# Kernel tuning notes

Measured on AMD Instinct MI355X. Metric: run time of the kernel, lower is better.

## Reference

```python
import jax, jax.numpy as jnp
import numpy as np

B, S, E, H, V = 64, 400, 512, 512, 32000


def setup_inputs() -> dict:
    key = jax.random.key(0)
    ks = jax.random.split(key, 16)
    sc = lambda fan: 1.0 / np.sqrt(fan)
    u = lambda k, shape, fan: jax.random.uniform(k, shape, jnp.float32, -sc(fan), sc(fan))
    mask = jax.random.randint(ks[3], (B, S), 0, 2).astype(bool)
    mask = mask.at[:, 0].set(True)  # ensure at least one valid position per row
    return {
        "decoder_input": jax.random.normal(ks[0], (B, E), jnp.float32),
        "previous_hidden_state": jax.random.normal(ks[1], (B, H), jnp.float32),
        "encoder_output": jax.random.normal(ks[2], (B, S, 2 * H), jnp.float32),
        "mask": mask,
        # GRUCell params (torch layout: weight_ih [3H,E], weight_hh [3H,H])
        "w_ih": u(ks[4], (3 * H, E), H),
        "w_hh": u(ks[5], (3 * H, H), H),
        "b_ih": u(ks[6], (3 * H,), H),
        "b_hh": u(ks[7], (3 * H,), H),
        # Attention params
        "Wh_w": u(ks[8], (H, 2 * H), 2 * H),
        "Wh_b": u(ks[9], (H,), 2 * H),
        "Ws_w": u(ks[10], (H, H), H),
        "Ws_b": u(ks[11], (H,), H),
        "vatt_w": u(ks[12], (1, H), H),  # Linear(H,1,bias=False)
        # Output projections
        "V_w": u(ks[13], (H, 3 * H), 3 * H),
        "V_b": u(ks[13], (H,), 3 * H),
        "Vhat_w": u(ks[14], (V, H), H),
        "Vhat_b": u(ks[15], (V,), H),
    }


def reference(decoder_input, previous_hidden_state, encoder_output, mask,
              w_ih, w_hh, b_ih, b_hh, Wh_w, Wh_b, Ws_w, Ws_b, vatt_w,
              V_w, V_b, Vhat_w, Vhat_b):
    # --- GRUCell step (torch semantics) ---
    gi = decoder_input @ w_ih.T + b_ih                  # [B, 3H]
    gh = previous_hidden_state @ w_hh.T + b_hh          # [B, 3H]
    i_r, i_z, i_n = jnp.split(gi, 3, axis=-1)
    h_r, h_z, h_n = jnp.split(gh, 3, axis=-1)
    r = jax.nn.sigmoid(i_r + h_r)
    z = jax.nn.sigmoid(i_z + h_z)
    n = jnp.tanh(i_n + r * h_n)
    hidden = (1.0 - z) * n + z * previous_hidden_state  # [B, H]

    # --- Additive (Bahdanau) attention ---
    feat = jnp.tanh(encoder_output @ Wh_w.T + Wh_b
                    + (hidden @ Ws_w.T + Ws_b)[:, None, :])   # [B, S, H]
    scores = jnp.einsum('bsh,h->bs', feat, vatt_w[0])          # [B, S]
    scores = jnp.where(mask, scores, -jnp.inf)
    attn_dist = jax.nn.softmax(scores, axis=-1)                # [B, S]

    # --- Context + output projection ---
    context_vector = jnp.einsum('bs,bsd->bd', attn_dist, encoder_output)  # [B, 2H]
    out = jnp.concatenate([hidden, context_vector], axis=-1) @ V_w.T + V_b  # [B, H]
    logits = out @ Vhat_w.T + Vhat_b                                        # [B, V]
    vocab_dist = jax.nn.softmax(logits, axis=-1)
    return (vocab_dist, attn_dist, context_vector, hidden)
```

## Files before the change

### kernel.cpp

```cpp
#include <hip/hip_runtime.h>
#include <hip/hip_bf16.h>
#include <stdint.h>

#define DI __device__ __forceinline__

using f32x4 = __attribute__((ext_vector_type(4))) float;
using s16x8 = __attribute__((ext_vector_type(8))) short;

#define BB 64
#define SS 400
#define HH 512
#define VVOC 32000
#define MTOT (BB*SS)

DI short bf16r(float f){
  __hip_bfloat16 h = __float2bfloat16(f);
  union { __hip_bfloat16 h; short s; } u; u.h = h; return u.s;
}
DI float sigm(float x){ return 1.f/(1.f + __expf(-x)); }
DI float tanhfast(float x){ x = fminf(x, 12.f); float e = __expf(2.f*x); return (e-1.f)/(e+1.f); }

DI void gload16b(const __hip_bfloat16* g, short* l){
  __builtin_amdgcn_global_load_lds(
      (const __attribute__((address_space(1))) __hip_bfloat16*)g,
      (__attribute__((address_space(3))) short*)l, 16, 0, 0);
}

DI float blkmax(float v, float* red, int t){
  #pragma unroll
  for (int o = 32; o; o >>= 1) v = fmaxf(v, __shfl_xor(v, o));
  if ((t & 63) == 0) red[t >> 6] = v;
  __syncthreads();
  v = fmaxf(fmaxf(red[0], red[1]), fmaxf(red[2], red[3]));
  __syncthreads();
  return v;
}
DI float blksum(float v, float* red, int t){
  #pragma unroll
  for (int o = 32; o; o >>= 1) v += __shfl_xor(v, o);
  if ((t & 63) == 0) red[t >> 6] = v;
  __syncthreads();
  v = red[0] + red[1] + red[2] + red[3];
  __syncthreads();
  return v;
}

DI s16x8 cvt8(const float* src){
  f32x4 a = ((const f32x4*)src)[0];
  f32x4 b = ((const f32x4*)src)[1];
  s16x8 o;
  o[0]=bf16r(a[0]); o[1]=bf16r(a[1]); o[2]=bf16r(a[2]); o[3]=bf16r(a[3]);
  o[4]=bf16r(b[0]); o[5]=bf16r(b[1]); o[6]=bf16r(b[2]); o[7]=bf16r(b[3]);
  return o;
}

DI s16x8 fragload16(const short* tile, int rbase, int kk, int l){
  int r = rbase + (l & 15);
  int c = (kk >> 3) + (l >> 4);
  int slot = c ^ (r & 7);
  return *(const s16x8*)(tile + r*64 + slot*8);
}

__global__ __launch_bounds__(256) void cvt_all(
    const float* __restrict__ enc, const float* __restrict__ wh,
    short* __restrict__ enc16, short* __restrict__ wh16,
    const unsigned int* __restrict__ mask, int mwords, int* __restrict__ flags)
{
  int b = blockIdx.x, t = threadIdx.x;
  if (b < 1600) {
    int i = b*256 + t;
    #pragma unroll
    for (int k = 0; k < 8; ++k) {
      int idx = i + k*409600;
      ((s16x8*)enc16)[idx] = cvt8(enc + (size_t)idx*8);
    }
  } else if (b < 1856) {
    int i = (b-1600)*256 + t;
    ((s16x8*)wh16)[i] = cvt8(wh + (size_t)i*8);
  } else {
    __shared__ int f;
    if (t == 0) f = 0;
    __syncthreads();
    int loc = 0;
    for (int i = (b-1856)*256 + t; i < mwords; i += 8*256) loc |= (mask[i] > 1u) ? 1 : 0;
    if (loc) atomicOr(&f, 1);
    __syncthreads();
    if (t == 0) flags[b-1856] = f;
  }
}

__global__ __launch_bounds__(256) void mfma_small(
    const float* __restrict__ A0, const float* __restrict__ A1,
    const float* __restrict__ W0, const float* __restrict__ W1,
    float* __restrict__ P0, float* __restrict__ P1,
    int K, int N)
{
  const float* A = blockIdx.z ? A1 : A0;
  const float* W = blockIdx.z ? W1 : W0;
  float*       P = blockIdx.z ? P1 : P0;
  __shared__ __align__(16) short lsa[64*64];
  __shared__ __align__(16) short lsb[64*64];
  const int t = threadIdx.x, l = t & 63, w = t >> 6;
  const int c0 = blockIdx.x*64;
  const int kbeg = blockIdx.y*64;

  #pragma unroll
  for (int q = 0; q < 2; ++q) {
    int it = q*256 + t;
    int r = it >> 3, c = it & 7;
    int slot = (c ^ (r & 7)) << 3;
    *(s16x8*)(lsa + r*64 + slot) = cvt8(A + (size_t)r*K + kbeg + c*8);
    *(s16x8*)(lsb + r*64 + slot) = cvt8(W + (size_t)(c0 + r)*K + kbeg + c*8);
  }
  __syncthreads();

  f32x4 acc[4];
  #pragma unroll
  for (int m = 0; m < 4; ++m) { f32x4 z = {0.f,0.f,0.f,0.f}; acc[m] = z; }
  #pragma unroll
  for (int kk = 0; kk < 64; kk += 32) {
    s16x8 bf = fragload16(lsb, w*16, kk, l);
    #pragma unroll
    for (int m = 0; m < 4; ++m) {
      s16x8 af = fragload16(lsa, m*16, kk, l);
      acc[m] = __builtin_amdgcn_mfma_f32_16x16x32_bf16(af, bf, acc[m], 0, 0, 0);
    }
  }
  const int kq = l >> 4, lc = l & 15;
  const int col = c0 + w*16 + lc;
  size_t pbase = (size_t)blockIdx.y * 64 * N;
  #pragma unroll
  for (int m = 0; m < 4; ++m)
    #pragma unroll
    for (int j = 0; j < 4; ++j)
      P[pbase + (size_t)(m*16 + kq*4 + j)*N + col] = acc[m][j];
}

__global__ __launch_bounds__(256) void score_gemm_bf16(
    const __hip_bfloat16* __restrict__ A, const __hip_bfloat16* __restrict__ Bw,
    const float* __restrict__ qv, const float* __restrict__ vb, float* __restrict__ dst)
{
  __shared__ __align__(16) short lsa[128*64];
  __shared__ __align__(16) short lsb[128*64];
  const int t = threadIdx.x;
  const int l = t & 63;
  const int w = t >> 6;
  const int wm = w >> 1, wn = w & 1;
  const int phys = blockIdx.x;
  const int logical = (phys & 7)*100 + (phys >> 3);
  const int mrow = (logical >> 2) * 128;
  const int colb = logical & 3;
  const int ncol = colb * 128;

  f32x4 acc[4][4];
  #pragma unroll
  for (int m = 0; m < 4; ++m)
    #pragma unroll
    for (int n = 0; n < 4; ++n) { f32x4 z = {0.f,0.f,0.f,0.f}; acc[m][n] = z; }

  for (int k0 = 0; k0 < 1024; k0 += 64) {
    #pragma unroll
    for (int i = 0; i < 4; ++i) {
      int ci = i*256 + t;
      int r = ci >> 3;
      int slot = ci & 7;
      int c = slot ^ (r & 7);
      gload16b(A + (size_t)(mrow + r)*1024 + k0 + c*8, lsa + ci*8);
      gload16b(Bw + (size_t)(ncol + r)*1024 + k0 + c*8, lsb + ci*8);
    }
    __syncthreads();
    #pragma unroll
    for (int kk = 0; kk < 64; kk += 32) {
      s16x8 bf[4];
      #pragma unroll
      for (int n = 0; n < 4; ++n) bf[n] = fragload16(lsb, wn*64 + n*16, kk, l);
      #pragma unroll
      for (int m = 0; m < 4; ++m) {
        s16x8 af = fragload16(lsa, wm*64 + m*16, kk, l);
        #pragma unroll
        for (int n = 0; n < 4; ++n)
          acc[m][n] = __builtin_amdgcn_mfma_f32_16x16x32_bf16(af, bf[n], acc[m][n], 0, 0, 0);
      }
    }
    __syncthreads();
  }

  const int kq = l >> 4, lc = l & 15;
  float vv[4];
  #pragma unroll
  for (int n = 0; n < 4; ++n) vv[n] = vb[ncol + wn*64 + n*16 + lc];
  #pragma unroll
  for (int m = 0; m < 4; ++m) {
    #pragma unroll
    for (int j = 0; j < 4; ++j) {
      int r = mrow + wm*64 + m*16 + kq*4 + j;
      int b = r / SS;
      const float* qb = qv + b*HH + ncol + wn*64 + lc;
      float ps = 0.f;
      #pragma unroll
      for (int n = 0; n < 4; ++n) ps += vv[n]*tanhfast(acc[m][n][j] + qb[n*16]);
      #pragma unroll
      for (int o = 1; o < 16; o <<= 1) ps += __shfl_xor(ps, o);
      if (lc == 0) dst[(colb*2 + wn)*MTOT + r] = ps;
    }
  }
}

__global__ __launch_bounds__(256) void vocab_gemm(
    const float* __restrict__ OUTm, const float* __restrict__ Vhat,
    const float* __restrict__ Vb, float* __restrict__ logits,
    float* __restrict__ MAXP, float* __restrict__ SUMP)
{
  __shared__ __align__(16) short lsa[64*64];
  __shared__ __align__(16) short lsb[64*64];
  __shared__ float red[64][8];
  const int t = threadIdx.x, l = t & 63, w = t >> 6;
  const int vrow0 = blockIdx.x * 64;

  f32x4 acc[4];
  #pragma unroll
  for (int m = 0; m < 4; ++m) { f32x4 z = {0.f,0.f,0.f,0.f}; acc[m] = z; }

  for (int k0 = 0; k0 < 512; k0 += 64) {
    #pragma unroll
    for (int q = 0; q < 2; ++q) {
      int it = q*256 + t;
      int r = it >> 3, c = it & 7;
      s16x8 o = cvt8(OUTm + (size_t)r*512 + k0 + c*8);
      *(s16x8*)(lsa + r*64 + ((c ^ (r & 7)) << 3)) = o;
    }
    #pragma unroll
    for (int q = 0; q < 2; ++q) {
      int it = q*256 + t;
      int r = it >> 3, c = it & 7;
      s16x8 o = cvt8(Vhat + (size_t)(vrow0 + r)*512 + k0 + c*8);
      *(s16x8*)(lsb + r*64 + ((c ^ (r & 7)) << 3)) = o;
    }
    __syncthreads();
    #pragma unroll
    for (int kk = 0; kk < 64; kk += 32) {
      s16x8 bf = fragload16(lsb, w*16, kk, l);
      #pragma unroll
      for (int m = 0; m < 4; ++m) {
        s16x8 af = fragload16(lsa, m*16, kk, l);
        acc[m] = __builtin_amdgcn_mfma_f32_16x16x32_bf16(af, bf, acc[m], 0, 0, 0);
      }
    }
    __syncthreads();
  }

  const int kq = l >> 4, lc = l & 15;
  const int voc = vrow0 + w*16 + lc;
  const float bias = Vb[voc];
  #pragma unroll
  for (int m = 0; m < 4; ++m)
    #pragma unroll
    for (int j = 0; j < 4; ++j) {
      acc[m][j] += bias;
      int brow = m*16 + kq*4 + j;
      logits[(size_t)brow*VVOC + voc] = acc[m][j];
    }
  #pragma unroll
  for (int m = 0; m < 4; ++m)
    #pragma unroll
    for (int j = 0; j < 4; ++j) {
      float v = acc[m][j];
      #pragma unroll
      for (int o = 1; o < 16; o <<= 1) v = fmaxf(v, __shfl_xor(v, o));
      if (lc == 0) red[m*16 + kq*4 + j][w] = v;
    }
  __syncthreads();
  float gmax[4][4];
  #pragma unroll
  for (int m = 0; m < 4; ++m)
    #pragma unroll
    for (int j = 0; j < 4; ++j) {
      int row = m*16 + kq*4 + j;
      gmax[m][j] = fmaxf(fmaxf(red[row][0], red[row][1]), fmaxf(red[row][2], red[row][3]));
    }
  __syncthreads();
  #pragma unroll
  for (int m = 0; m < 4; ++m)
    #pragma unroll
    for (int j = 0; j < 4; ++j) {
      float s = __expf(acc[m][j] - gmax[m][j]);
      #pragma unroll
      for (int o = 1; o < 16; o <<= 1) s += __shfl_xor(s, o);
      if (lc == 0) red[m*16 + kq*4 + j][4 + w] = s;
    }
  __syncthreads();
  if (t < 64) {
    float M = fmaxf(fmaxf(red[t][0], red[t][1]), fmaxf(red[t][2], red[t][3]));
    float S = red[t][4] + red[t][5] + red[t][6] + red[t][7];
    MAXP[blockIdx.x*64 + t] = M;
    SUMP[blockIdx.x*64 + t] = S;
  }
}

__global__ __launch_bounds__(256) void vnorm(
    const float* __restrict__ MAXP, const float* __restrict__ SUMP,
    float* __restrict__ logits)
{
  __shared__ float red[4];
  int b = blockIdx.x, q = blockIdx.y, t = threadIdx.x;
  float m = -INFINITY;
  for (int i = t; i < 500; i += 256) m = fmaxf(m, MAXP[i*64 + b]);
  m = blkmax(m, red, t);
  float z = 0.f;
  for (int i = t; i < 500; i += 256) z += SUMP[i*64 + b] * __expf(MAXP[i*64 + b] - m);
  z = blksum(z, red, t);
  float inv = 1.f / z;
  f32x4* p = (f32x4*)(logits + (size_t)b*VVOC + q*8000);
  for (int i = t; i < 2000; i += 256) {
    f32x4 v = p[i];
    #pragma unroll
    for (int c = 0; c < 4; ++c) v[c] = __expf(v[c] - m) * inv;
    p[i] = v;
  }
}

__global__ void combineN(const float* __restrict__ P, const float* __restrict__ b1,
                         const float* __restrict__ b2, float* __restrict__ dstv,
                         int N, int total, int nseg)
{
  int i = blockIdx.x*256 + threadIdx.x;
  if (i >= total) return;
  float a = 0.f;
  for (int s = 0; s < nseg; ++s) a += P[(size_t)s*total + i];
  int c = i % N;
  if (b1) a += b1[c];
  if (b2) a += b2[c];
  dstv[i] = a;
}

__global__ void gru_gate(const float* __restrict__ GI, const float* __restrict__ GH,
                         const float* __restrict__ b_ih, const float* __restrict__ b_hh,
                         const float* __restrict__ hprev, float* __restrict__ hid,
                         float* __restrict__ concat)
{
  int i = blockIdx.x*256 + threadIdx.x;
  int b = i >> 9, h = i & 511;
  float ir=0, iz=0, inn=0, hr=0, hz=0, hn=0;
  #pragma unroll
  for (int s = 0; s < 8; ++s) {
    const float* gi = GI + (size_t)s*(64*1536) + b*1536;
    const float* gh = GH + (size_t)s*(64*1536) + b*1536;
    ir += gi[h];      iz += gi[512+h];  inn += gi[1024+h];
    hr += gh[h];      hz += gh[512+h];  hn  += gh[1024+h];
  }
  ir += b_ih[h]; iz += b_ih[512+h]; inn += b_ih[1024+h];
  hr += b_hh[h]; hz += b_hh[512+h]; hn  += b_hh[1024+h];
  float r = sigm(ir + hr), z = sigm(iz + hz);
  float n = tanhfast(inn + r*hn);
  float hv = (1.f - z)*n + z*hprev[i];
  hid[i] = hv;
  concat[b*1536 + h] = hv;
}

__global__ void softmax_s(const float* __restrict__ part, const void* __restrict__ mask,
                          const int* __restrict__ flags, float* __restrict__ attn)
{
  __shared__ float red[4];
  int b = blockIdx.x, t = threadIdx.x;
  bool isbyte = (flags[0]|flags[1]|flags[2]|flags[3]|flags[4]|flags[5]|flags[6]|flags[7]) != 0;
  float sc0, sc1 = -INFINITY;
  {
    float v = 0.f;
    #pragma unroll
    for (int p = 0; p < 8; ++p) v += part[p*MTOT + b*SS + t];
    bool mv = isbyte ? (((const unsigned char*)mask)[b*SS + t] != 0)
                     : (((const int*)mask)[b*SS + t] != 0);
    sc0 = mv ? v : -INFINITY;
  }
  int s1 = t + 256;
  if (s1 < SS) {
    float v = 0.f;
    #pragma unroll
    for (int p = 0; p < 8; ++p) v += part[p*MTOT + b*SS + s1];
    bool mv = isbyte ? (((const unsigned char*)mask)[b*SS + s1] != 0)
                     : (((const int*)mask)[b*SS + s1] != 0);
    sc1 = mv ? v : -INFINITY;
  }
  float mx = blkmax(fmaxf(sc0, sc1), red, t);
  float e0 = __expf(sc0 - mx), e1 = __expf(sc1 - mx);
  float sum = blksum(e0 + e1, red, t);
  float inv = 1.f / sum;
  attn[b*SS + t] = e0 * inv;
  if (s1 < SS) attn[b*SS + s1] = e1 * inv;
}

__global__ void ctx_part(const float* __restrict__ attn, const unsigned int* __restrict__ enc16,
                         float* __restrict__ CTXP)
{
  int b = blockIdx.x, dh = blockIdx.y, sq = blockIdx.z;
  int d0 = dh*512 + threadIdx.x*2;
  const float* a = attn + b*SS + sq*50;
  const unsigned int* e = enc16 + (((size_t)(b*SS + sq*50)*1024 + d0) >> 1);
  float lo = 0.f, hi = 0.f;
  #pragma unroll 5
  for (int s = 0; s < 50; ++s) {
    unsigned int u = e[(size_t)s*512];
    float av = a[s];
    lo += av * __uint_as_float(u << 16);
    hi += av * __uint_as_float(u & 0xffff0000u);
  }
  float* dst = CTXP + (size_t)sq*65536 + b*1024 + d0;
  dst[0] = lo; dst[1] = hi;
}

__global__ void ctx_combine(const float* __restrict__ CTXP, float* __restrict__ ctx,
                            float* __restrict__ concat)
{
  int b = blockIdx.x;
  for (int d = threadIdx.x; d < 1024; d += 256) {
    float s = 0.f;
    #pragma unroll
    for (int q = 0; q < 8; ++q) s += CTXP[q*65536 + b*1024 + d];
    ctx[b*1024 + d] = s;
    concat[b*1536 + 512 + d] = s;
  }
}

extern "C" void kernel_launch(void* const* d_in, const int* in_sizes, int n_in,
                              void* d_out, int out_size, void* d_ws, size_t ws_size,
                              hipStream_t stream) {
  (void)in_sizes; (void)n_in; (void)out_size; (void)ws_size;
  const float* x      = (const float*)d_in[0];
  const float* hprev  = (const float*)d_in[1];
  const float* enc    = (const float*)d_in[2];
  const void*  mask   = d_in[3];
  const float* w_ih   = (const float*)d_in[4];
  const float* w_hh   = (const float*)d_in[5];
  const float* b_ih   = (const float*)d_in[6];
  const float* b_hh   = (const float*)d_in[7];
  const float* Wh_w   = (const float*)d_in[8];
  const float* Wh_b   = (const float*)d_in[9];
  const float* Ws_w   = (const float*)d_in[10];
  const float* Ws_b   = (const float*)d_in[11];
  const float* vatt   = (const float*)d_in[12];
  const float* V_w    = (const float*)d_in[13];
  const float* V_b    = (const float*)d_in[14];
  const float* Vhat_w = (const float*)d_in[15];
  const float* Vhat_b = (const float*)d_in[16];

  float* out   = (float*)d_out;
  float* vocab = out;
  float* attn  = out + 2048000;
  float* ctx   = out + 2073600;
  float* hid   = out + 2139136;

  float* WS     = (float*)d_ws;
  int*   FLAGS  = (int*)d_ws;
  float* GI     = WS + 16;
  float* GH     = GI + 786432;
  float* QP     = GH + 786432;
  float* Q      = QP + 262144;
  float* OUT    = Q + 32768;
  float* PART   = OUT + 32768;
  float* MAXP   = PART + 204800;
  float* SUMP   = MAXP + 32000;
  float* CTXP   = SUMP + 32000;
  float* OUTP   = CTXP + 524288;
  float* CONCAT = OUTP + 786432;
  float* ENDF   = CONCAT + 98304;
  size_t f32_bytes = ((size_t)((char*)ENDF - (char*)d_ws) + 15) & ~(size_t)15;
  short* ENC16 = (short*)((char*)d_ws + f32_bytes);
  short* WH16  = ENC16 + (size_t)25600*1024;

  cvt_all<<<dim3(1864), 256, 0, stream>>>(enc, Wh_w, ENC16, WH16,
                                          (const unsigned int*)mask, 6400, FLAGS);
  mfma_small<<<dim3(24, 8, 2), 256, 0, stream>>>(x, hprev, w_ih, w_hh, GI, GH, 512, 1536);
  gru_gate<<<dim3(128), 256, 0, stream>>>(GI, GH, b_ih, b_hh, hprev, hid, CONCAT);
  mfma_small<<<dim3(8, 8, 1), 256, 0, stream>>>(hid, hid, Ws_w, Ws_w, QP, QP, 512, 512);
  combineN<<<dim3(128), 256, 0, stream>>>(QP, Ws_b, Wh_b, Q, 512, 32768, 8);
  score_gemm_bf16<<<dim3(800), 256, 0, stream>>>(
      (const __hip_bfloat16*)ENC16, (const __hip_bfloat16*)WH16, Q, vatt, PART);
  softmax_s<<<dim3(64), 256, 0, stream>>>(PART, mask, FLAGS, attn);
  ctx_part<<<dim3(64, 2, 8), 256, 0, stream>>>(attn, (const unsigned int*)ENC16, CTXP);
  ctx_combine<<<dim3(64), 256, 0, stream>>>(CTXP, ctx, CONCAT);
  mfma_small<<<dim3(8, 24, 1), 256, 0, stream>>>(CONCAT, CONCAT, V_w, V_w, OUTP, OUTP, 1536, 512);
  combineN<<<dim3(128), 256, 0, stream>>>(OUTP, V_b, nullptr, OUT, 512, 32768, 24);
  vocab_gemm<<<dim3(500), 256, 0, stream>>>(OUT, Vhat_w, Vhat_b, vocab, MAXP, SUMP);
  vnorm<<<dim3(64, 4), 256, 0, stream>>>(MAXP, SUMP, vocab);
}
```

Baseline: 157.8 us.

## Fuse pre-GEMMs into conversion kernel, fuse GRU gate with query, widen score tiles

Folds the GRU input/hidden GEMMs into the bf16 conversion launch as extra blocks, and merges the GRU gate and the Ws query projection into one per-batch kernel that computes the query with fp32 dot products from shared memory. The score GEMM now uses 512-thread blocks with 128x256 tiles so each encoder tile is reused across more columns. The vocab GEMM register-prefetches the next K slice before converting the current one. Together these cut kernel launches and global round trips. The cost is more LDS and registers in the score kernel, and a fused_hidq grid of only 64 blocks.

```diff
diff --git a/kernel.cpp b/kernel.cpp
--- a/kernel.cpp
+++ b/kernel.cpp
@@ -45,13 +45,14 @@
   return v;
 }
 
-DI s16x8 cvt8(const float* src){
-  f32x4 a = ((const f32x4*)src)[0];
-  f32x4 b = ((const f32x4*)src)[1];
+DI s16x8 cvt8v(f32x4 a, f32x4 b){
   s16x8 o;
   o[0]=bf16r(a[0]); o[1]=bf16r(a[1]); o[2]=bf16r(a[2]); o[3]=bf16r(a[3]);
   o[4]=bf16r(b[0]); o[5]=bf16r(b[1]); o[6]=bf16r(b[2]); o[7]=bf16r(b[3]);
   return o;
+}
+DI s16x8 cvt8(const float* src){
+  return cvt8v(((const f32x4*)src)[0], ((const f32x4*)src)[1]);
 }
 
 DI s16x8 fragload16(const short* tile, int rbase, int kk, int l){
@@ -61,11 +62,52 @@
   return *(const s16x8*)(tile + r*64 + slot*8);
 }
 
-__global__ __launch_bounds__(256) void cvt_all(
+DI void mfma_small_body(const float* __restrict__ A, const float* __restrict__ W,
+                        float* __restrict__ P, int K, int N, int c0, int kseg,
+                        short* lsa, short* lsb, int t)
+{
+  const int kbeg = kseg*64;
+  const int l = t & 63, w = t >> 6;
+  #pragma unroll
+  for (int q = 0; q < 2; ++q) {
+    int it = q*256 + t;
+    int r = it >> 3, c = it & 7;
+    int slot = (c ^ (r & 7)) << 3;
+    *(s16x8*)(lsa + r*64 + slot) = cvt8(A + (size_t)r*K + kbeg + c*8);
+    *(s16x8*)(lsb + r*64 + slot) = cvt8(W + (size_t)(c0 + r)*K + kbeg + c*8);
+  }
+  __syncthreads();
+  f32x4 acc[4];
+  #pragma unroll
+  for (int m = 0; m < 4; ++m) { f32x4 z = {0.f,0.f,0.f,0.f}; acc[m] = z; }
+  #pragma unroll
+  for (int kk = 0; kk < 64; kk += 32) {
+    s16x8 bf = fragload16(lsb, w*16, kk, l);
+    #pragma unroll
+    for (int m = 0; m < 4; ++m) {
+      s16x8 af = fragload16(lsa, m*16, kk, l);
+      acc[m] = __builtin_amdgcn_mfma_f32_16x16x32_bf16(af, bf, acc[m], 0, 0, 0);
+    }
+  }
+  const int kq = l >> 4, lc = l & 15;
+  const int col = c0 + w*16 + lc;
+  size_t pbase = (size_t)kseg * 64 * N;
+  #pragma unroll
+  for (int m = 0; m < 4; ++m)
+    #pragma unroll
+    for (int j = 0; j < 4; ++j)
+      P[pbase + (size_t)(m*16 + kq*4 + j)*N + col] = acc[m][j];
+}
+
+__global__ __launch_bounds__(256) void k_pre(
     const float* __restrict__ enc, const float* __restrict__ wh,
     short* __restrict__ enc16, short* __restrict__ wh16,
-    const unsigned int* __restrict__ mask, int mwords, int* __restrict__ flags)
-{
+    const unsigned int* __restrict__ mask, int mwords, int* __restrict__ flags,
+    const float* __restrict__ x, const float* __restrict__ hprev,
+    const float* __restrict__ w_ih, const float* __restrict__ w_hh,
+    float* __restrict__ GI, float* __restrict__ GH)
+{
+  __shared__ __align__(16) short ls[2][64*64];
   int b = blockIdx.x, t = threadIdx.x;
   if (b < 1600) {
     int i = b*256 + t;
@@ -77,7 +119,7 @@
   } else if (b < 1856) {
     int i = (b-1600)*256 + t;
     ((s16x8*)wh16)[i] = cvt8(wh + (size_t)i*8);
-  } else {
+  } else if (b < 1864) {
     __shared__ int f;
     if (t == 0) f = 0;
     __syncthreads();
@@ -86,71 +128,73 @@
     if (loc) atomicOr(&f, 1);
     __syncthreads();
     if (t == 0) flags[b-1856] = f;
-  }
-}
-
-__global__ __launch_bounds__(256) void mfma_small(
-    const float* __restrict__ A0, const float* __restrict__ A1,
-    const float* __restrict__ W0, const float* __restrict__ W1,
-    float* __restrict__ P0, float* __restrict__ P1,
-    int K, int N)
-{
-  const float* A = blockIdx.z ? A1 : A0;
-  const float* W = blockIdx.z ? W1 : W0;
-  float*       P = blockIdx.z ? P1 : P0;
-  __shared__ __align__(16) short lsa[64*64];
-  __shared__ __align__(16) short lsb[64*64];
-  const int t = threadIdx.x, l = t & 63, w = t >> 6;
-  const int c0 = blockIdx.x*64;
-  const int kbeg = blockIdx.y*64;
-
-  #pragma unroll
-  for (int q = 0; q < 2; ++q) {
-    int it = q*256 + t;
-    int r = it >> 3, c = it & 7;
-    int slot = (c ^ (r & 7)) << 3;
-    *(s16x8*)(lsa + r*64 + slot) = cvt8(A + (size_t)r*K + kbeg + c*8);
-    *(s16x8*)(lsb + r*64 + slot) = cvt8(W + (size_t)(c0 + r)*K + kbeg + c*8);
-  }
-  __syncthreads();
-
-  f32x4 acc[4];
-  #pragma unroll
-  for (int m = 0; m < 4; ++m) { f32x4 z = {0.f,0.f,0.f,0.f}; acc[m] = z; }
-  #pragma unroll
-  for (int kk = 0; kk < 64; kk += 32) {
-    s16x8 bf = fragload16(lsb, w*16, kk, l);
-    #pragma unroll
-    for (int m = 0; m < 4; ++m) {
-      s16x8 af = fragload16(lsa, m*16, kk, l);
-      acc[m] = __builtin_amdgcn_mfma_f32_16x16x32_bf16(af, bf, acc[m], 0, 0, 0);
-    }
-  }
-  const int kq = l >> 4, lc = l & 15;
-  const int col = c0 + w*16 + lc;
-  size_t pbase = (size_t)blockIdx.y * 64 * N;
-  #pragma unroll
-  for (int m = 0; m < 4; ++m)
-    #pragma unroll
-    for (int j = 0; j < 4; ++j)
-      P[pbase + (size_t)(m*16 + kq*4 + j)*N + col] = acc[m][j];
-}
-
-__global__ __launch_bounds__(256) void score_gemm_bf16(
+  } else {
+    int gb = b - 1864;
+    int colI = gb % 24;
+    int kseg = (gb / 24) % 8;
+    int z    = gb / 192;
+    mfma_small_body(z ? hprev : x, z ? w_hh : w_ih, z ? GH : GI,
+                    512, 1536, colI*64, kseg, ls[0], ls[1], t);
+  }
+}
+
+__global__ __launch_bounds__(256) void fused_hidq(
+    const float* __restrict__ GI, const float* __restrict__ GH,
+    const float* __restrict__ b_ih, const float* __restrict__ b_hh,
+    const float* __restrict__ hprev, const float* __restrict__ Ws_w,
+    const float* __restrict__ Ws_b, const float* __restrict__ Wh_b,
+    float* __restrict__ hid, float* __restrict__ concat, float* __restrict__ Q)
+{
+  __shared__ float sh[512];
+  int b = blockIdx.x, t = threadIdx.x;
+  for (int h = t; h < 512; h += 256) {
+    float ir=0, iz=0, inn=0, hr=0, hz=0, hn=0;
+    #pragma unroll
+    for (int s = 0; s < 8; ++s) {
+      const float* gi = GI + (size_t)s*(64*1536) + b*1536;
+      const float* gh = GH + (size_t)s*(64*1536) + b*1536;
+      ir += gi[h];      iz += gi[512+h];  inn += gi[1024+h];
+      hr += gh[h];      hz += gh[512+h];  hn  += gh[1024+h];
+    }
+    ir += b_ih[h]; iz += b_ih[512+h]; inn += b_ih[1024+h];
+    hr += b_hh[h]; hz += b_hh[512+h]; hn  += b_hh[1024+h];
+    float r = sigm(ir + hr), z = sigm(iz + hz);
+    float n = tanhfast(inn + r*hn);
+    float hv = (1.f - z)*n + z*hprev[b*512 + h];
+    hid[b*512 + h] = hv;
+    concat[b*1536 + h] = hv;
+    sh[h] = hv;
+  }
+  __syncthreads();
+  for (int c = t; c < 512; c += 256) {
+    const f32x4* wrow = (const f32x4*)(Ws_w + (size_t)c*512);
+    float a0=0.f, a1=0.f, a2=0.f, a3=0.f;
+    #pragma unroll 8
+    for (int k4 = 0; k4 < 128; ++k4) {
+      f32x4 wv = wrow[k4];
+      f32x4 hv = *(const f32x4*)(sh + k4*4);
+      a0 += wv[0]*hv[0]; a1 += wv[1]*hv[1]; a2 += wv[2]*hv[2]; a3 += wv[3]*hv[3];
+    }
+    Q[b*512 + c] = (a0+a1)+(a2+a3) + Ws_b[c] + Wh_b[c];
+  }
+}
+
+__global__ __launch_bounds__(512) void score_gemm_bf16(
     const __hip_bfloat16* __restrict__ A, const __hip_bfloat16* __restrict__ Bw,
     const float* __restrict__ qv, const float* __restrict__ vb, float* __restrict__ dst)
 {
   __shared__ __align__(16) short lsa[128*64];
-  __shared__ __align__(16) short lsb[128*64];
+  __shared__ __align__(16) short lsb[256*64];
   const int t = threadIdx.x;
   const int l = t & 63;
   const int w = t >> 6;
-  const int wm = w >> 1, wn = w & 1;
+  const int wm = w >> 2;
+  const int wn = w & 3;
   const int phys = blockIdx.x;
-  const int logical = (phys & 7)*100 + (phys >> 3);
-  const int mrow = (logical >> 2) * 128;
-  const int colb = logical & 3;
-  const int ncol = colb * 128;
+  const int logical = (phys & 7)*50 + (phys >> 3);
+  const int mrow = (logical >> 1) * 128;
+  const int colb = logical & 1;
+  const int ncol = colb * 256;
 
   f32x4 acc[4][4];
   #pragma unroll
@@ -160,12 +204,17 @@
 
   for (int k0 = 0; k0 < 1024; k0 += 64) {
     #pragma unroll
-    for (int i = 0; i < 4; ++i) {
-      int ci = i*256 + t;
-      int r = ci >> 3;
-      int slot = ci & 7;
+    for (int i = 0; i < 2; ++i) {
+      int ci = i*512 + t;
+      int r = ci >> 3, slot = ci & 7;
       int c = slot ^ (r & 7);
       gload16b(A + (size_t)(mrow + r)*1024 + k0 + c*8, lsa + ci*8);
+    }
+    #pragma unroll
+    for (int i = 0; i < 4; ++i) {
+      int ci = i*512 + t;
+      int r = ci >> 3, slot = ci & 7;
+      int c = slot ^ (r & 7);
       gload16b(Bw + (size_t)(ncol + r)*1024 + k0 + c*8, lsb + ci*8);
     }
     __syncthreads();
@@ -189,6 +238,7 @@
   float vv[4];
   #pragma unroll
   for (int n = 0; n < 4; ++n) vv[n] = vb[ncol + wn*64 + n*16 + lc];
+  const int seg = colb*4 + wn;
   #pragma unroll
   for (int m = 0; m < 4; ++m) {
     #pragma unroll
@@ -201,7 +251,7 @@
       for (int n = 0; n < 4; ++n) ps += vv[n]*tanhfast(acc[m][n][j] + qb[n*16]);
       #pragma unroll
       for (int o = 1; o < 16; o <<= 1) ps += __shfl_xor(ps, o);
-      if (lc == 0) dst[(colb*2 + wn)*MTOT + r] = ps;
+      if (lc == 0) dst[seg*MTOT + r] = ps;
     }
   }
 }
@@ -221,33 +271,48 @@
   #pragma unroll
   for (int m = 0; m < 4; ++m) { f32x4 z = {0.f,0.f,0.f,0.f}; acc[m] = z; }
 
-  for (int k0 = 0; k0 < 512; k0 += 64) {
-    #pragma unroll
-    for (int q = 0; q < 2; ++q) {
-      int it = q*256 + t;
-      int r = it >> 3, c = it & 7;
-      s16x8 o = cvt8(OUTm + (size_t)r*512 + k0 + c*8);
-      *(s16x8*)(lsa + r*64 + ((c ^ (r & 7)) << 3)) = o;
-    }
-    #pragma unroll
-    for (int q = 0; q < 2; ++q) {
-      int it = q*256 + t;
-      int r = it >> 3, c = it & 7;
-      s16x8 o = cvt8(Vhat + (size_t)(vrow0 + r)*512 + k0 + c*8);
-      *(s16x8*)(lsb + r*64 + ((c ^ (r & 7)) << 3)) = o;
-    }
+  f32x4 pa0[2][2], pb0[2][2], pa1[2][2], pb1[2][2];
+
+  #define VLOAD(pa, pb, k0)                                                     \
+    _Pragma("unroll")                                                           \
+    for (int q = 0; q < 2; ++q) {                                               \
+      int it = q*256 + t; int r = it >> 3, c = it & 7;                          \
+      const f32x4* ap = (const f32x4*)(OUTm + (size_t)r*512 + (k0) + c*8);      \
+      pa[q][0] = ap[0]; pa[q][1] = ap[1];                                       \
+      const f32x4* bp = (const f32x4*)(Vhat + (size_t)(vrow0 + r)*512 + (k0) + c*8); \
+      pb[q][0] = bp[0]; pb[q][1] = bp[1];                                       \
+    }
+  #define VSTEP(pa, pb)                                                         \
+    _Pragma("unroll")                                                           \
+    for (int q = 0; q < 2; ++q) {                                               \
+      int it = q*256 + t; int r = it >> 3, c = it & 7;                          \
+      int slot = (c ^ (r & 7)) << 3;                                            \
+      *(s16x8*)(lsa + r*64 + slot) = cvt8v(pa[q][0], pa[q][1]);                 \
+      *(s16x8*)(lsb + r*64 + slot) = cvt8v(pb[q][0], pb[q][1]);                 \
+    }                                                                           \
+    __syncthreads();                                                            \
+    _Pragma("unroll")                                                           \
+    for (int kk = 0; kk < 64; kk += 32) {                                       \
+      s16x8 bf = fragload16(lsb, w*16, kk, l);                                  \
+      _Pragma("unroll")                                                         \
+      for (int m = 0; m < 4; ++m) {                                             \
+        s16x8 af = fragload16(lsa, m*16, kk, l);                                \
+        acc[m] = __builtin_amdgcn_mfma_f32_16x16x32_bf16(af, bf, acc[m], 0,0,0);\
+      }                                                                         \
+    }                                                                           \
     __syncthreads();
-    #pragma unroll
-    for (int kk = 0; kk < 64; kk += 32) {
-      s16x8 bf = fragload16(lsb, w*16, kk, l);
-      #pragma unroll
-      for (int m = 0; m < 4; ++m) {
-        s16x8 af = fragload16(lsa, m*16, kk, l);
-        acc[m] = __builtin_amdgcn_mfma_f32_16x16x32_bf16(af, bf, acc[m], 0, 0, 0);
-      }
-    }
-    __syncthreads();
-  }
+
+  VLOAD(pa0, pb0, 0)
+  #pragma unroll
+  for (int s2 = 0; s2 < 4; ++s2) {
+    int k0 = s2*128;
+    if (k0 + 64 < 512) { VLOAD(pa1, pb1, k0 + 64) }
+    VSTEP(pa0, pb0)
+    if (k0 + 128 < 512) { VLOAD(pa0, pb0, k0 + 128) }
+    VSTEP(pa1, pb1)
+  }
+  #undef VLOAD
+  #undef VSTEP
 
   const int kq = l >> 4, lc = l & 15;
   const int voc = vrow0 + w*16 + lc;
@@ -257,8 +322,7 @@
     #pragma unroll
     for (int j = 0; j < 4; ++j) {
       acc[m][j] += bias;
-      int brow = m*16 + kq*4 + j;
-      logits[(size_t)brow*VVOC + voc] = acc[m][j];
+      logits[(size_t)(m*16 + kq*4 + j)*VVOC + voc] = acc[m][j];
     }
   #pragma unroll
   for (int m = 0; m < 4; ++m)
@@ -319,42 +383,23 @@
   }
 }
 
+__global__ __launch_bounds__(256) void mfma_small(
+    const float* __restrict__ A, const float* __restrict__ W,
+    float* __restrict__ P, int K, int N)
+{
+  __shared__ __align__(16) short ls[2][64*64];
+  mfma_small_body(A, W, P, K, N, blockIdx.x*64, blockIdx.y, ls[0], ls[1], threadIdx.x);
+}
+
 __global__ void combineN(const float* __restrict__ P, const float* __restrict__ b1,
-                         const float* __restrict__ b2, float* __restrict__ dstv,
-                         int N, int total, int nseg)
+                         float* __restrict__ dstv, int N, int total, int nseg)
 {
   int i = blockIdx.x*256 + threadIdx.x;
   if (i >= total) return;
   float a = 0.f;
   for (int s = 0; s < nseg; ++s) a += P[(size_t)s*total + i];
-  int c = i % N;
-  if (b1) a += b1[c];
-  if (b2) a += b2[c];
+  if (b1) a += b1[i % N];
   dstv[i] = a;
-}
-
-__global__ void gru_gate(const float* __restrict__ GI, const float* __restrict__ GH,
-                         const float* __restrict__ b_ih, const float* __restrict__ b_hh,
-                         const float* __restrict__ hprev, float* __restrict__ hid,
-                         float* __restrict__ concat)
-{
-  int i = blockIdx.x*256 + threadIdx.x;
-  int b = i >> 9, h = i & 511;
-  float ir=0, iz=0, inn=0, hr=0, hz=0, hn=0;
-  #pragma unroll
-  for (int s = 0; s < 8; ++s) {
-    const float* gi = GI + (size_t)s*(64*1536) + b*1536;
-    const float* gh = GH + (size_t)s*(64*1536) + b*1536;
-    ir += gi[h];      iz += gi[512+h];  inn += gi[1024+h];
-    hr += gh[h];      hz += gh[512+h];  hn  += gh[1024+h];
-  }
-  ir += b_ih[h]; iz += b_ih[512+h]; inn += b_ih[1024+h];
-  hr += b_hh[h]; hz += b_hh[512+h]; hn  += b_hh[1024+h];
-  float r = sigm(ir + hr), z = sigm(iz + hz);
-  float n = tanhfast(inn + r*hn);
-  float hv = (1.f - z)*n + z*hprev[i];
-  hid[i] = hv;
-  concat[b*1536 + h] = hv;
 }
 
 __global__ void softmax_s(const float* __restrict__ part, const void* __restrict__ mask,
@@ -453,8 +498,7 @@
   int*   FLAGS  = (int*)d_ws;
   float* GI     = WS + 16;
   float* GH     = GI + 786432;
-  float* QP     = GH + 786432;
-  float* Q      = QP + 262144;
+  float* Q      = GH + 786432;
   float* OUT    = Q + 32768;
   float* PART   = OUT + 32768;
   float* MAXP   = PART + 204800;
@@ -467,19 +511,18 @@
   short* ENC16 = (short*)((char*)d_ws + f32_bytes);
   short* WH16  = ENC16 + (size_t)25600*1024;
 
-  cvt_all<<<dim3(1864), 256, 0, stream>>>(enc, Wh_w, ENC16, WH16,
-                                          (const unsigned int*)mask, 6400, FLAGS);
-  mfma_small<<<dim3(24, 8, 2), 256, 0, stream>>>(x, hprev, w_ih, w_hh, GI, GH, 512, 1536);
-  gru_gate<<<dim3(128), 256, 0, stream>>>(GI, GH, b_ih, b_hh, hprev, hid, CONCAT);
-  mfma_small<<<dim3(8, 8, 1), 256, 0, stream>>>(hid, hid, Ws_w, Ws_w, QP, QP, 512, 512);
-  combineN<<<dim3(128), 256, 0, stream>>>(QP, Ws_b, Wh_b, Q, 512, 32768, 8);
-  score_gemm_bf16<<<dim3(800), 256, 0, stream>>>(
+  k_pre<<<dim3(2248), 256, 0, stream>>>(enc, Wh_w, ENC16, WH16,
+                                        (const unsigned int*)mask, 6400, FLAGS,
+                                        x, hprev, w_ih, w_hh, GI, GH);
+  fused_hidq<<<dim3(64), 256, 0, stream>>>(GI, GH, b_ih, b_hh, hprev,
+                                           Ws_w, Ws_b, Wh_b, hid, CONCAT, Q);
+  score_gemm_bf16<<<dim3(400), 512, 0, stream>>>(
       (const __hip_bfloat16*)ENC16, (const __hip_bfloat16*)WH16, Q, vatt, PART);
   softmax_s<<<dim3(64), 256, 0, stream>>>(PART, mask, FLAGS, attn);
   ctx_part<<<dim3(64, 2, 8), 256, 0, stream>>>(attn, (const unsigned int*)ENC16, CTXP);
   ctx_combine<<<dim3(64), 256, 0, stream>>>(CTXP, ctx, CONCAT);
-  mfma_small<<<dim3(8, 24, 1), 256, 0, stream>>>(CONCAT, CONCAT, V_w, V_w, OUTP, OUTP, 1536, 512);
-  combineN<<<dim3(128), 256, 0, stream>>>(OUTP, V_b, nullptr, OUT, 512, 32768, 24);
+  mfma_small<<<dim3(8, 24), 256, 0, stream>>>(CONCAT, V_w, OUTP, 1536, 512);
+  combineN<<<dim3(128), 256, 0, stream>>>(OUTP, V_b, OUT, 512, 32768, 24);
   vocab_gemm<<<dim3(500), 256, 0, stream>>>(OUT, Vhat_w, Vhat_b, vocab, MAXP, SUMP);
   vnorm<<<dim3(64, 4), 256, 0, stream>>>(MAXP, SUMP, vocab);
 }
```

After: 160.6 us. About the same (+1.7%).
